# Performance work log

Hardware: AMD Instinct MI355X
Metric: run time of the kernel (lower is better)

The kernel has to match this reference:

```python
import jax, jax.numpy as jnp
import numpy as np
from jax import lax

B, N, C = 8, 100000, 90
H = W = 512
CONF_THR = 0.25
IOU_THR = 0.45
MAX_DET = 100  # fixed-size padded replacement for dynamic per-image NMS output


def setup_inputs() -> dict:
    key = jax.random.key(0)
    k1, k2, k3, k4, k5 = jax.random.split(key, 5)
    # small deltas so exp(dw), exp(dh) stay sane
    regression = jax.random.normal(k1, (B, N, 4), jnp.float32) * 0.1
    # shifted logits so sigmoid scores are mostly below conf_threshold (realistic sparsity)
    classification = jax.random.normal(k2, (B, N, C), jnp.float32) * 2.0 - 4.0
    # anchors in (y1, x1, y2, x2), valid boxes inside a 512x512 canvas
    cy = jax.random.uniform(k3, (1, N), minval=0.0, maxval=float(H))
    cx = jax.random.uniform(k4, (1, N), minval=0.0, maxval=float(W))
    hw = jax.random.uniform(k5, (1, N, 2), minval=16.0, maxval=128.0)
    hh, ww = hw[..., 0], hw[..., 1]
    anchors = jnp.stack([cy - hh / 2, cx - ww / 2, cy + hh / 2, cx + ww / 2], axis=-1)
    imgs = jnp.zeros((B, 3, H, W), jnp.float32)  # only shape (H, W) is used
    return {"regression": regression, "classification": classification,
            "anchors": anchors, "imgs": imgs}


def _bbox_transform(anchors, regression):
    y_c_a = (anchors[..., 0] + anchors[..., 2]) / 2
    x_c_a = (anchors[..., 1] + anchors[..., 3]) / 2
    ha = anchors[..., 2] - anchors[..., 0]
    wa = anchors[..., 3] - anchors[..., 1]
    w = jnp.exp(regression[..., 3]) * wa
    h = jnp.exp(regression[..., 2]) * ha
    y_c = regression[..., 0] * ha + y_c_a
    x_c = regression[..., 1] * wa + x_c_a
    # output in (x1, y1, x2, y2)
    return jnp.stack([x_c - w / 2, y_c - h / 2, x_c + w / 2, y_c + h / 2], axis=-1)


def _clip_boxes(boxes, height, width):
    x = jnp.clip(boxes[..., 0::2], 0.0, float(width))
    y = jnp.clip(boxes[..., 1::2], 0.0, float(height))
    return jnp.stack([x[..., 0], y[..., 0], x[..., 1], y[..., 1]], axis=-1)


def _iou_one_vs_all(box, boxes):
    # box [4], boxes [N,4] in x1y1x2y2
    x1 = jnp.maximum(box[0], boxes[:, 0])
    y1 = jnp.maximum(box[1], boxes[:, 1])
    x2 = jnp.minimum(box[2], boxes[:, 2])
    y2 = jnp.minimum(box[3], boxes[:, 3])
    inter = jnp.clip(x2 - x1, 0.0) * jnp.clip(y2 - y1, 0.0)
    area = (box[2] - box[0]) * (box[3] - box[1])
    areas = (boxes[:, 2] - boxes[:, 0]) * (boxes[:, 3] - boxes[:, 1])
    return inter / (area + areas - inter + 1e-8)


def _process_image(boxes, cls_logits):
    # boxes [N,4], cls_logits [N,C]
    scores_all = jax.nn.sigmoid(cls_logits)
    max_scores = jnp.max(scores_all, axis=1)
    labels = jnp.argmax(scores_all, axis=1)
    # below-threshold anchors get -1 so they can never be selected (== torch pre-NMS filter)
    s0 = jnp.where(max_scores > CONF_THR, max_scores, -1.0)
    s0 = lax.stop_gradient(s0)
    boxes_sg = lax.stop_gradient(boxes)

    def step(sc, _):
        best = jnp.argmax(sc)
        valid = sc[best] > 0.0
        iou = _iou_one_vs_all(boxes_sg[best], boxes_sg)
        sc = jnp.where(valid & (iou > IOU_THR), -1.0, sc)
        sc = sc.at[best].set(-1.0)
        return sc, jnp.where(valid, best, -1)

    _, idx = lax.scan(step, s0, None, length=MAX_DET)  # [MAX_DET] int
    valid = idx >= 0
    idx_safe = jnp.maximum(idx, 0)
    out_scores = jnp.where(valid, max_scores[idx_safe], 0.0)
    out_labels = jnp.where(valid, labels[idx_safe], -1)
    out_boxes = jnp.where(valid[:, None], boxes[idx_safe], 0.0)
    return out_scores, out_labels, out_boxes


def reference(regression, classification, anchors, imgs):
    height, width = imgs.shape[2], imgs.shape[3]
    boxes = _bbox_transform(anchors, regression)          # [B,N,4]
    boxes = _clip_boxes(boxes, height, width)
    scores, labels, det_boxes = jax.vmap(_process_image)(boxes, classification)
    # padded outputs: scores [B,MAX_DET], labels [B,MAX_DET] (-1 = invalid), boxes [B,MAX_DET,4]
    return scores, labels, det_boxes
```

## Files before the change

### kernel.cpp

```cpp
#include <hip/hip_runtime.h>

#define NB 8
#define NA 100000
#define NC 90
#define MAXDET 100
#define KCAND 2048
#define NBINS 4096
#define NBLK 13
#define BLK_ANCH 8000
#define CONF 0.25f
#define IOUT 0.45f

static constexpr size_t OFF_BOX   = 0;
static constexpr size_t OFF_SCORE = OFF_BOX   + (size_t)NB * NA * 16;
static constexpr size_t OFF_LABEL = OFF_SCORE + (size_t)NB * NA * 4;
static constexpr size_t OFF_HROWS = OFF_LABEL + (size_t)NB * NA;
static constexpr size_t OFF_THR   = OFF_HROWS + (size_t)NB * NBLK * NBINS * 4;
static constexpr size_t OFF_CNT   = OFF_THR   + 64;
static constexpr size_t OFF_CKEY  = OFF_CNT   + 64;
static constexpr size_t OFF_CBOX  = OFF_CKEY  + (size_t)NB * KCAND * 8;
static constexpr size_t OFF_CLAB  = OFF_CBOX  + (size_t)NB * KCAND * 16;

__device__ __forceinline__ float4 decode_clip(float4 a, float4 r) {
#pragma clang fp contract(off)
    float yca = (a.x + a.z) * 0.5f;
    float xca = (a.y + a.w) * 0.5f;
    float ha  = a.z - a.x;
    float wa  = a.w - a.y;
    float w   = expf(r.w) * wa;
    float h   = expf(r.z) * ha;
    float yc  = r.x * ha + yca;
    float xc  = r.y * wa + xca;
    float x1  = xc - w * 0.5f, y1 = yc - h * 0.5f;
    float x2  = xc + w * 0.5f, y2 = yc + h * 0.5f;
    x1 = fminf(fmaxf(x1, 0.0f), 512.0f);
    x2 = fminf(fmaxf(x2, 0.0f), 512.0f);
    y1 = fminf(fmaxf(y1, 0.0f), 512.0f);
    y2 = fminf(fmaxf(y2, 0.0f), 512.0f);
    return make_float4(x1, y1, x2, y2);
}

__global__ __launch_bounds__(256) void k_score_box(const float* __restrict__ cls,
                                                   const float* __restrict__ reg,
                                                   const float* __restrict__ anc,
                                                   float4* __restrict__ ws_box,
                                                   float* __restrict__ ws_score,
                                                   unsigned char* __restrict__ ws_label) {
    int tid = threadIdx.x;
    int grp = tid >> 4;
    int lane = tid & 15;
    int a_idx = blockIdx.x * 16 + grp;

    const float* p = cls + (size_t)a_idx * NC;
    unsigned long long best = 0ULL;
#pragma unroll
    for (int t = 0; t < 6; ++t) {
        int j = lane + 16 * t;
        if (j < NC) {
            float x = p[j];
            float s = 1.0f / (1.0f + expf(-x));
            unsigned long long key = ((unsigned long long)__float_as_uint(s) << 32) |
                                     (unsigned long long)(unsigned)(NC - 1 - j);
            if (key > best) best = key;
        }
    }
#pragma unroll
    for (int off = 8; off >= 1; off >>= 1) {
        unsigned long long o = __shfl_xor(best, off, 16);
        if (o > best) best = o;
    }
    if (lane == 0) {
        ws_score[a_idx] = __uint_as_float((unsigned)(best >> 32));
        ws_label[a_idx] = (unsigned char)(NC - 1 - (int)(best & 0xFFFFFFFFu));
    }

    if (tid < 16) {
        int idx = blockIdx.x * 16 + tid;
        int n = idx % NA;
        float4 a = ((const float4*)anc)[n];
        float4 r = ((const float4*)reg)[idx];
        ws_box[idx] = decode_clip(a, r);
    }
}

__global__ __launch_bounds__(256) void k_hist(const float* __restrict__ ws_score,
                                              unsigned* __restrict__ hrows) {
    __shared__ unsigned h[NBINS];
    int b = blockIdx.y, blk = blockIdx.x, tid = threadIdx.x;
    for (int i = tid; i < NBINS; i += 256) h[i] = 0u;
    __syncthreads();
    int base = blk * BLK_ANCH;
    int lim = min(BLK_ANCH, NA - base);
    const float* sc = ws_score + (size_t)b * NA + base;
    for (int i = tid; i < lim; i += 256) {
        float s = sc[i];
        if (s > CONF) {
            int bin = min((int)(s * (float)NBINS), NBINS - 1);
            atomicAdd(&h[bin], 1u);
        }
    }
    __syncthreads();
    unsigned* row = hrows + ((size_t)b * NBLK + blk) * NBINS;
    for (int i = tid; i < NBINS; i += 256) row[i] = h[i];
}

__global__ __launch_bounds__(256) void k_thresh(const unsigned* __restrict__ hrows,
                                                unsigned* __restrict__ thr_bin,
                                                unsigned* __restrict__ cnt) {
    __shared__ unsigned h[NBINS];
    __shared__ unsigned chunk[256];
    __shared__ int bstar;
    int b = blockIdx.x, t = threadIdx.x;
    for (int i = t; i < NBINS; i += 256) {
        unsigned s = 0;
        for (int r = 0; r < NBLK; ++r) s += hrows[((size_t)b * NBLK + r) * NBINS + i];
        h[i] = s;
    }
    if (t == 0) { bstar = NBINS - 1; cnt[b] = 0u; }
    __syncthreads();
    unsigned s = 0;
    for (int j = 0; j < 16; ++j) s += h[t * 16 + j];
    chunk[t] = s;
    __syncthreads();
    unsigned U = 0;
    for (int j = t + 1; j < 256; ++j) U += chunk[j];
    unsigned run = U;
    int cand = NBINS;
    for (int j = 15; j >= 0; --j) {
        run += h[t * 16 + j];
        if (run <= (unsigned)KCAND) cand = t * 16 + j;
    }
    if (cand < NBINS) atomicMin(&bstar, cand);
    __syncthreads();
    if (t == 0) thr_bin[b] = (unsigned)bstar;
}

__global__ __launch_bounds__(256) void k_compact(const float* __restrict__ ws_score,
                                                 const unsigned char* __restrict__ ws_label,
                                                 const float4* __restrict__ ws_box,
                                                 const unsigned* __restrict__ thr_bin,
                                                 unsigned* __restrict__ cnt,
                                                 unsigned long long* __restrict__ ckey,
                                                 float4* __restrict__ cbox,
                                                 int* __restrict__ clab) {
    __shared__ unsigned scan[256];
    __shared__ unsigned base_s;
    int b = blockIdx.y, blk = blockIdx.x, t = threadIdx.x;
    int base = blk * BLK_ANCH;
    int lim = min(BLK_ANCH, NA - base);
    size_t ibase = (size_t)b * NA + base;
    unsigned thr = thr_bin[b];

    unsigned c = 0;
    for (int i = t; i < lim; i += 256) {
        float s = ws_score[ibase + i];
        if (s > CONF) {
            int bin = min((int)(s * (float)NBINS), NBINS - 1);
            if ((unsigned)bin >= thr) c++;
        }
    }
    scan[t] = c;
    __syncthreads();
    for (int off = 1; off < 256; off <<= 1) {
        unsigned v = (t >= off) ? scan[t - off] : 0u;
        __syncthreads();
        scan[t] += v;
        __syncthreads();
    }
    if (t == 255) base_s = atomicAdd(&cnt[b], scan[255]);
    __syncthreads();
    unsigned pos = base_s + scan[t] - c;
    for (int i = t; i < lim; i += 256) {
        float s = ws_score[ibase + i];
        if (s > CONF) {
            int bin = min((int)(s * (float)NBINS), NBINS - 1);
            if ((unsigned)bin >= thr) {
                unsigned p = pos++;
                if (p < (unsigned)KCAND) {
                    int n = base + i;
                    ckey[(size_t)b * KCAND + p] =
                        ((unsigned long long)__float_as_uint(s) << 32) |
                        (unsigned long long)(0xFFFFFFFFu - (unsigned)n);
                    cbox[(size_t)b * KCAND + p] = ws_box[ibase + i];
                    clab[(size_t)b * KCAND + p] = (int)ws_label[ibase + i];
                }
            }
        }
    }
}

__global__ __launch_bounds__(256) void k_nms(const unsigned long long* __restrict__ ckey,
                                             const float4* __restrict__ cbox,
                                             const int* __restrict__ clab,
                                             const unsigned* __restrict__ cnt,
                                             float* __restrict__ out) {
    __shared__ unsigned long long key[KCAND];
    __shared__ float4 box[KCAND];
    __shared__ int lab[KCAND];
    __shared__ unsigned long long bestkey;
    __shared__ float4 bestbox;
    __shared__ int bestlab;
    __shared__ float out_s[MAXDET];
    __shared__ float out_l[MAXDET];
    __shared__ float4 out_b[MAXDET];

    int b = blockIdx.x, t = threadIdx.x;
    unsigned M = min(cnt[b], (unsigned)KCAND);
    for (int j = t; j < KCAND; j += 256) {
        if (j < (int)M) {
            key[j] = ckey[b * KCAND + j];
            box[j] = cbox[b * KCAND + j];
            lab[j] = clab[b * KCAND + j];
        } else {
            key[j] = 0ULL;
        }
    }
    if (t == 0) bestkey = 0ULL;
    __syncthreads();

    for (int k = 0; k < MAXDET; ++k) {
        unsigned long long m = 0ULL;
#pragma unroll
        for (int s = 0; s < KCAND / 256; ++s) {
            unsigned long long v = key[t + s * 256];
            if (v > m) m = v;
        }
#pragma unroll
        for (int off = 32; off >= 1; off >>= 1) {
            unsigned long long o = __shfl_xor(m, off, 64);
            if (o > m) m = o;
        }
        if ((t & 63) == 0) atomicMax(&bestkey, m);
        __syncthreads();
        unsigned long long bk = bestkey;
        if (bk) {
#pragma unroll
            for (int s = 0; s < KCAND / 256; ++s) {
                int j = t + s * 256;
                if (key[j] == bk) {
                    bestbox = box[j];
                    bestlab = lab[j];
                    key[j] = 0ULL;
                }
            }
        }
        __syncthreads();
        if (bk) {
#pragma clang fp contract(off)
            float4 bb = bestbox;
            float areaB = (bb.z - bb.x) * (bb.w - bb.y);
#pragma unroll
            for (int s = 0; s < KCAND / 256; ++s) {
                int j = t + s * 256;
                unsigned long long kj = key[j];
                if (kj) {
                    float4 bj = box[j];
                    float x1 = fmaxf(bb.x, bj.x), y1 = fmaxf(bb.y, bj.y);
                    float x2 = fminf(bb.z, bj.z), y2 = fminf(bb.w, bj.w);
                    float inter = fmaxf(x2 - x1, 0.0f) * fmaxf(y2 - y1, 0.0f);
                    float areaJ = (bj.z - bj.x) * (bj.w - bj.y);
                    float iou = inter / (areaB + areaJ - inter + 1e-8f);
                    if (iou > IOUT) key[j] = 0ULL;
                }
            }
        }
        if (t == 0) {
            if (bk) {
                out_s[k] = __uint_as_float((unsigned)(bk >> 32));
                out_l[k] = (float)bestlab;
                out_b[k] = bestbox;
            } else {
                out_s[k] = 0.0f;
                out_l[k] = -1.0f;
                out_b[k] = make_float4(0.f, 0.f, 0.f, 0.f);
            }
            bestkey = 0ULL;
        }
        __syncthreads();
    }

    if (t < MAXDET) {
        out[b * MAXDET + t] = out_s[t];
        out[NB * MAXDET + b * MAXDET + t] = out_l[t];
    }
    for (int j = t; j < MAXDET * 4; j += 256) {
        int d = j >> 2, c = j & 3;
        float4 bb = out_b[d];
        float v = (c == 0) ? bb.x : (c == 1) ? bb.y : (c == 2) ? bb.z : bb.w;
        out[2 * NB * MAXDET + (size_t)(b * MAXDET + d) * 4 + c] = v;
    }
}

extern "C" void kernel_launch(void* const* d_in, const int* in_sizes, int n_in,
                              void* d_out, int out_size, void* d_ws, size_t ws_size,
                              hipStream_t stream) {
    const float* reg = (const float*)d_in[0];
    const float* cls = (const float*)d_in[1];
    const float* anc = (const float*)d_in[2];

    char* ws = (char*)d_ws;
    float4* ws_box            = (float4*)(ws + OFF_BOX);
    float* ws_score           = (float*)(ws + OFF_SCORE);
    unsigned char* ws_label   = (unsigned char*)(ws + OFF_LABEL);
    unsigned* hrows           = (unsigned*)(ws + OFF_HROWS);
    unsigned* thr_bin         = (unsigned*)(ws + OFF_THR);
    unsigned* cnt             = (unsigned*)(ws + OFF_CNT);
    unsigned long long* ckey  = (unsigned long long*)(ws + OFF_CKEY);
    float4* cbox              = (float4*)(ws + OFF_CBOX);
    int* clab                 = (int*)(ws + OFF_CLAB);

    float* out = (float*)d_out;

    k_score_box<<<NB * NA / 16, 256, 0, stream>>>(cls, reg, anc, ws_box, ws_score, ws_label);
    k_hist<<<dim3(NBLK, NB), 256, 0, stream>>>(ws_score, hrows);
    k_thresh<<<NB, 256, 0, stream>>>(hrows, thr_bin, cnt);
    k_compact<<<dim3(NBLK, NB), 256, 0, stream>>>(ws_score, ws_label, ws_box, thr_bin, cnt,
                                                  ckey, cbox, clab);
    k_nms<<<NB, 256, 0, stream>>>(ckey, cbox, clab, cnt, out);
}
```

Measured before the change: 694.1 us.

## Replace greedy NMS with sorted bitmask NMS and lazy box decode

The score kernel now stages classification rows in shared memory and uses two threads per anchor. Box decoding is moved out of the full pass and done only for the compacted candidates after a bitonic sort. NMS becomes a parallel IoU bitmask build over all candidate pairs, followed by a sequential scan over the sorted mask with double-buffered chunk loads. The aim is to remove the per-anchor decode traffic and the 100 serial argmax rounds. In exchange it adds two kernel launches and a 2048x2048 IoU mask computation.

```diff
diff --git a/kernel.cpp b/kernel.cpp
--- a/kernel.cpp
+++ b/kernel.cpp
@@ -8,18 +8,22 @@
 #define NBINS 4096
 #define NBLK 13
 #define BLK_ANCH 8000
+#define ABLK 128
+#define MASK_WORDS 32
+#define CH_ROWS 64
 #define CONF 0.25f
 #define IOUT 0.45f
 
-static constexpr size_t OFF_BOX   = 0;
-static constexpr size_t OFF_SCORE = OFF_BOX   + (size_t)NB * NA * 16;
+static constexpr size_t OFF_SCORE = 0;
 static constexpr size_t OFF_LABEL = OFF_SCORE + (size_t)NB * NA * 4;
 static constexpr size_t OFF_HROWS = OFF_LABEL + (size_t)NB * NA;
 static constexpr size_t OFF_THR   = OFF_HROWS + (size_t)NB * NBLK * NBINS * 4;
-static constexpr size_t OFF_CNT   = OFF_THR   + 64;
-static constexpr size_t OFF_CKEY  = OFF_CNT   + 64;
-static constexpr size_t OFF_CBOX  = OFF_CKEY  + (size_t)NB * KCAND * 8;
-static constexpr size_t OFF_CLAB  = OFF_CBOX  + (size_t)NB * KCAND * 16;
+static constexpr size_t OFF_CNT   = OFF_THR + 64;
+static constexpr size_t OFF_CKEY  = OFF_CNT + 64;
+static constexpr size_t OFF_SSC   = OFF_CKEY + (size_t)NB * KCAND * 8;
+static constexpr size_t OFF_SLAB  = OFF_SSC + (size_t)NB * KCAND * 4;
+static constexpr size_t OFF_SBOX  = OFF_SLAB + (size_t)NB * KCAND * 4;
+static constexpr size_t OFF_MASK  = OFF_SBOX + (size_t)NB * KCAND * 16;
 
 __device__ __forceinline__ float4 decode_clip(float4 a, float4 r) {
 #pragma clang fp contract(off)
@@ -41,45 +45,32 @@
 }
 
 __global__ __launch_bounds__(256) void k_score_box(const float* __restrict__ cls,
-                                                   const float* __restrict__ reg,
-                                                   const float* __restrict__ anc,
-                                                   float4* __restrict__ ws_box,
                                                    float* __restrict__ ws_score,
                                                    unsigned char* __restrict__ ws_label) {
-    int tid = threadIdx.x;
-    int grp = tid >> 4;
-    int lane = tid & 15;
-    int a_idx = blockIdx.x * 16 + grp;
-
-    const float* p = cls + (size_t)a_idx * NC;
+    __shared__ float tile[ABLK * NC];
+    int t = threadIdx.x;
+    const float4* g4 = (const float4*)(cls + (size_t)blockIdx.x * (ABLK * NC));
+    float4* t4 = (float4*)tile;
+    for (int i = t; i < ABLK * NC / 4; i += 256) t4[i] = g4[i];
+    __syncthreads();
+
+    int la = t >> 1, h = t & 1;
+    const float* row = tile + la * NC + h * 45;
+    int jbase = NC - 1 - h * 45;
     unsigned long long best = 0ULL;
-#pragma unroll
-    for (int t = 0; t < 6; ++t) {
-        int j = lane + 16 * t;
-        if (j < NC) {
-            float x = p[j];
-            float s = 1.0f / (1.0f + expf(-x));
-            unsigned long long key = ((unsigned long long)__float_as_uint(s) << 32) |
-                                     (unsigned long long)(unsigned)(NC - 1 - j);
-            if (key > best) best = key;
-        }
-    }
-#pragma unroll
-    for (int off = 8; off >= 1; off >>= 1) {
-        unsigned long long o = __shfl_xor(best, off, 16);
-        if (o > best) best = o;
-    }
-    if (lane == 0) {
-        ws_score[a_idx] = __uint_as_float((unsigned)(best >> 32));
-        ws_label[a_idx] = (unsigned char)(NC - 1 - (int)(best & 0xFFFFFFFFu));
-    }
-
-    if (tid < 16) {
-        int idx = blockIdx.x * 16 + tid;
-        int n = idx % NA;
-        float4 a = ((const float4*)anc)[n];
-        float4 r = ((const float4*)reg)[idx];
-        ws_box[idx] = decode_clip(a, r);
+    for (int j2 = 0; j2 < 45; ++j2) {
+        float x = row[j2];
+        float s = 1.0f / (1.0f + expf(-x));
+        unsigned long long key = ((unsigned long long)__float_as_uint(s) << 32) |
+                                 (unsigned long long)(unsigned)(jbase - j2);
+        if (key > best) best = key;
+    }
+    unsigned long long o = __shfl_xor(best, 1, 64);
+    if (o > best) best = o;
+    if (h == 0) {
+        int a = blockIdx.x * ABLK + la;
+        ws_score[a] = __uint_as_float((unsigned)(best >> 32));
+        ws_label[a] = (unsigned char)(NC - 1 - (unsigned)(best & 0xFFFFFFFFu));
     }
 }
 
@@ -136,13 +127,9 @@
 }
 
 __global__ __launch_bounds__(256) void k_compact(const float* __restrict__ ws_score,
-                                                 const unsigned char* __restrict__ ws_label,
-                                                 const float4* __restrict__ ws_box,
                                                  const unsigned* __restrict__ thr_bin,
                                                  unsigned* __restrict__ cnt,
-                                                 unsigned long long* __restrict__ ckey,
-                                                 float4* __restrict__ cbox,
-                                                 int* __restrict__ clab) {
+                                                 unsigned long long* __restrict__ ckey) {
     __shared__ unsigned scan[256];
     __shared__ unsigned base_s;
     int b = blockIdx.y, blk = blockIdx.x, t = threadIdx.x;
@@ -181,113 +168,163 @@
                     ckey[(size_t)b * KCAND + p] =
                         ((unsigned long long)__float_as_uint(s) << 32) |
                         (unsigned long long)(0xFFFFFFFFu - (unsigned)n);
-                    cbox[(size_t)b * KCAND + p] = ws_box[ibase + i];
-                    clab[(size_t)b * KCAND + p] = (int)ws_label[ibase + i];
                 }
             }
         }
     }
 }
 
-__global__ __launch_bounds__(256) void k_nms(const unsigned long long* __restrict__ ckey,
-                                             const float4* __restrict__ cbox,
-                                             const int* __restrict__ clab,
-                                             const unsigned* __restrict__ cnt,
-                                             float* __restrict__ out) {
+__global__ __launch_bounds__(256) void k_sortdecode(const unsigned long long* __restrict__ ckey,
+                                                    const unsigned* __restrict__ cnt,
+                                                    const unsigned char* __restrict__ ws_label,
+                                                    const float* __restrict__ reg,
+                                                    const float* __restrict__ anc,
+                                                    float* __restrict__ sscore,
+                                                    int* __restrict__ slab,
+                                                    float4* __restrict__ sbox) {
     __shared__ unsigned long long key[KCAND];
-    __shared__ float4 box[KCAND];
-    __shared__ int lab[KCAND];
-    __shared__ unsigned long long bestkey;
-    __shared__ float4 bestbox;
-    __shared__ int bestlab;
-    __shared__ float out_s[MAXDET];
-    __shared__ float out_l[MAXDET];
-    __shared__ float4 out_b[MAXDET];
-
     int b = blockIdx.x, t = threadIdx.x;
     unsigned M = min(cnt[b], (unsigned)KCAND);
-    for (int j = t; j < KCAND; j += 256) {
-        if (j < (int)M) {
-            key[j] = ckey[b * KCAND + j];
-            box[j] = cbox[b * KCAND + j];
-            lab[j] = clab[b * KCAND + j];
-        } else {
-            key[j] = 0ULL;
-        }
-    }
-    if (t == 0) bestkey = 0ULL;
-    __syncthreads();
-
-    for (int k = 0; k < MAXDET; ++k) {
-        unsigned long long m = 0ULL;
-#pragma unroll
-        for (int s = 0; s < KCAND / 256; ++s) {
-            unsigned long long v = key[t + s * 256];
-            if (v > m) m = v;
-        }
-#pragma unroll
-        for (int off = 32; off >= 1; off >>= 1) {
-            unsigned long long o = __shfl_xor(m, off, 64);
-            if (o > m) m = o;
-        }
-        if ((t & 63) == 0) atomicMax(&bestkey, m);
-        __syncthreads();
-        unsigned long long bk = bestkey;
-        if (bk) {
-#pragma unroll
+    for (int i = t; i < KCAND; i += 256)
+        key[i] = (i < (int)M) ? ckey[(size_t)b * KCAND + i] : 0ULL;
+    __syncthreads();
+    for (int k = 2; k <= KCAND; k <<= 1) {
+        for (int j = k >> 1; j > 0; j >>= 1) {
             for (int s = 0; s < KCAND / 256; ++s) {
-                int j = t + s * 256;
-                if (key[j] == bk) {
-                    bestbox = box[j];
-                    bestlab = lab[j];
-                    key[j] = 0ULL;
+                int p = t + s * 256;
+                int q = p ^ j;
+                if (q > p) {
+                    unsigned long long a = key[p], bb = key[q];
+                    bool desc = ((p & k) == 0);
+                    if (desc ? (a < bb) : (a > bb)) { key[p] = bb; key[q] = a; }
                 }
             }
-        }
-        __syncthreads();
-        if (bk) {
+            __syncthreads();
+        }
+    }
+    for (int i = t; i < KCAND; i += 256) {
+        unsigned long long kk = key[i];
+        size_t o = (size_t)b * KCAND + i;
+        if (kk != 0ULL) {
+            unsigned n = 0xFFFFFFFFu - (unsigned)(kk & 0xFFFFFFFFu);
+            sscore[o] = __uint_as_float((unsigned)(kk >> 32));
+            slab[o] = (int)ws_label[(size_t)b * NA + n];
+            float4 a4 = ((const float4*)anc)[n];
+            float4 r4 = ((const float4*)reg)[(size_t)b * NA + n];
+            sbox[o] = decode_clip(a4, r4);
+        } else {
+            sscore[o] = 0.0f;
+            slab[o] = -1;
+            sbox[o] = make_float4(0.f, 0.f, 0.f, 0.f);
+        }
+    }
+}
+
+__global__ __launch_bounds__(256) void k_mask(const float4* __restrict__ sbox,
+                                              unsigned long long* __restrict__ mask) {
+    __shared__ float4 bx[KCAND];
+    int b = blockIdx.y, t = threadIdx.x;
+    for (int i = t; i < KCAND; i += 256) bx[i] = sbox[(size_t)b * KCAND + i];
+    __syncthreads();
+    int r = t >> 5, w = t & 31;
+    int row = blockIdx.x * 8 + r;
+    float4 rb = bx[row];
+    unsigned long long bits = 0ULL;
+    {
 #pragma clang fp contract(off)
-            float4 bb = bestbox;
-            float areaB = (bb.z - bb.x) * (bb.w - bb.y);
+        float areaR = (rb.z - rb.x) * (rb.w - rb.y);
+        int cbase = w * 64;
+        for (int cc = 0; cc < 64; ++cc) {
+            float4 cb = bx[cbase + cc];
+            float x1 = fmaxf(rb.x, cb.x), y1 = fmaxf(rb.y, cb.y);
+            float x2 = fminf(rb.z, cb.z), y2 = fminf(rb.w, cb.w);
+            float inter = fmaxf(x2 - x1, 0.0f) * fmaxf(y2 - y1, 0.0f);
+            float areaC = (cb.z - cb.x) * (cb.w - cb.y);
+            float iou = inter / (areaR + areaC - inter + 1e-8f);
+            if (iou > IOUT) bits |= (1ULL << cc);
+        }
+    }
+    mask[((size_t)b * KCAND + row) * MASK_WORDS + w] = bits;
+}
+
+__global__ __launch_bounds__(256) void k_scan(const unsigned long long* __restrict__ mask,
+                                              const unsigned* __restrict__ cnt,
+                                              const float* __restrict__ sscore,
+                                              const int* __restrict__ slab,
+                                              const float4* __restrict__ sbox,
+                                              float* __restrict__ out) {
+    __shared__ unsigned long long buf[2][CH_ROWS * MASK_WORDS];
+    __shared__ int picks[MAXDET];
+    __shared__ int npick_s;
+    __shared__ int done_s;
+
+    int b = blockIdx.x, t = threadIdx.x;
+    unsigned M = min(cnt[b], (unsigned)KCAND);
+    const unsigned long long* mbase = mask + (size_t)b * KCAND * MASK_WORDS;
+
+    if (t == 0) { npick_s = 0; done_s = 0; }
+    for (int i = t; i < CH_ROWS * MASK_WORDS; i += 256) buf[0][i] = mbase[i];
+    __syncthreads();
+
+    unsigned long long removed = 0ULL;
+    int npick = 0;
+
+    for (int q = 0; q < KCAND / CH_ROWS; ++q) {
+        int cur = q & 1;
+        bool havepre = (q + 1 < KCAND / CH_ROWS) && !done_s;
+        unsigned long long pre[CH_ROWS * MASK_WORDS / 256];
+        if (havepre) {
+            const unsigned long long* src = mbase + (size_t)(q + 1) * CH_ROWS * MASK_WORDS;
 #pragma unroll
-            for (int s = 0; s < KCAND / 256; ++s) {
-                int j = t + s * 256;
-                unsigned long long kj = key[j];
-                if (kj) {
-                    float4 bj = box[j];
-                    float x1 = fmaxf(bb.x, bj.x), y1 = fmaxf(bb.y, bj.y);
-                    float x2 = fminf(bb.z, bj.z), y2 = fminf(bb.w, bj.w);
-                    float inter = fmaxf(x2 - x1, 0.0f) * fmaxf(y2 - y1, 0.0f);
-                    float areaJ = (bj.z - bj.x) * (bj.w - bj.y);
-                    float iou = inter / (areaB + areaJ - inter + 1e-8f);
-                    if (iou > IOUT) key[j] = 0ULL;
+            for (int s = 0; s < CH_ROWS * MASK_WORDS / 256; ++s) pre[s] = src[t + s * 256];
+        }
+        if (t < 64) {
+            const unsigned long long* ch = buf[cur];
+            int gstart = q * 64;
+            if (gstart < (int)M && npick < MAXDET) {
+                int vg = (int)M - gstart;
+                unsigned long long valid = (vg >= 64) ? ~0ULL : ((1ULL << vg) - 1ULL);
+                while (npick < MAXDET) {
+                    unsigned long long rg = __shfl(removed, q, 64);
+                    unsigned long long free = ~rg & valid;
+                    if (free == 0ULL) break;
+                    int cl = __ffsll((long long)free) - 1;
+                    int c = gstart + cl;
+                    if (t == 0) picks[npick] = c;
+                    npick++;
+                    if (t == q) removed |= (1ULL << cl);
+                    if (t < 32) removed |= ch[cl * MASK_WORDS + t];
                 }
             }
-        }
-        if (t == 0) {
-            if (bk) {
-                out_s[k] = __uint_as_float((unsigned)(bk >> 32));
-                out_l[k] = (float)bestlab;
-                out_b[k] = bestbox;
-            } else {
-                out_s[k] = 0.0f;
-                out_l[k] = -1.0f;
-                out_b[k] = make_float4(0.f, 0.f, 0.f, 0.f);
+            if (t == 0) {
+                npick_s = npick;
+                done_s = (npick >= MAXDET || (q + 1) * CH_ROWS >= (int)M) ? 1 : 0;
             }
-            bestkey = 0ULL;
+        }
+        if (havepre) {
+#pragma unroll
+            for (int s = 0; s < CH_ROWS * MASK_WORDS / 256; ++s)
+                buf[1 - cur][t + s * 256] = pre[s];
         }
         __syncthreads();
-    }
-
-    if (t < MAXDET) {
-        out[b * MAXDET + t] = out_s[t];
-        out[NB * MAXDET + b * MAXDET + t] = out_l[t];
-    }
-    for (int j = t; j < MAXDET * 4; j += 256) {
-        int d = j >> 2, c = j & 3;
-        float4 bb = out_b[d];
-        float v = (c == 0) ? bb.x : (c == 1) ? bb.y : (c == 2) ? bb.z : bb.w;
-        out[2 * NB * MAXDET + (size_t)(b * MAXDET + d) * 4 + c] = v;
+        if (done_s) break;
+    }
+
+    __syncthreads();
+    int np = npick_s;
+    for (int k = t; k < MAXDET; k += 256) {
+        float sc = 0.0f, lb = -1.0f;
+        float4 bb = make_float4(0.f, 0.f, 0.f, 0.f);
+        if (k < np) {
+            int i = picks[k];
+            size_t o = (size_t)b * KCAND + i;
+            sc = sscore[o];
+            lb = (float)slab[o];
+            bb = sbox[o];
+        }
+        out[b * MAXDET + k] = sc;
+        out[NB * MAXDET + b * MAXDET + k] = lb;
+        ((float4*)(out + 2 * NB * MAXDET))[b * MAXDET + k] = bb;
     }
 }
 
@@ -299,22 +336,24 @@
     const float* anc = (const float*)d_in[2];
 
     char* ws = (char*)d_ws;
-    float4* ws_box            = (float4*)(ws + OFF_BOX);
     float* ws_score           = (float*)(ws + OFF_SCORE);
     unsigned char* ws_label   = (unsigned char*)(ws + OFF_LABEL);
     unsigned* hrows           = (unsigned*)(ws + OFF_HROWS);
     unsigned* thr_bin         = (unsigned*)(ws + OFF_THR);
     unsigned* cnt             = (unsigned*)(ws + OFF_CNT);
     unsigned long long* ckey  = (unsigned long long*)(ws + OFF_CKEY);
-    float4* cbox              = (float4*)(ws + OFF_CBOX);
-    int* clab                 = (int*)(ws + OFF_CLAB);
+    float* sscore             = (float*)(ws + OFF_SSC);
+    int* slab                 = (int*)(ws + OFF_SLAB);
+    float4* sbox              = (float4*)(ws + OFF_SBOX);
+    unsigned long long* maskp = (unsigned long long*)(ws + OFF_MASK);
 
     float* out = (float*)d_out;
 
-    k_score_box<<<NB * NA / 16, 256, 0, stream>>>(cls, reg, anc, ws_box, ws_score, ws_label);
+    k_score_box<<<NB * NA / ABLK, 256, 0, stream>>>(cls, ws_score, ws_label);
     k_hist<<<dim3(NBLK, NB), 256, 0, stream>>>(ws_score, hrows);
     k_thresh<<<NB, 256, 0, stream>>>(hrows, thr_bin, cnt);
-    k_compact<<<dim3(NBLK, NB), 256, 0, stream>>>(ws_score, ws_label, ws_box, thr_bin, cnt,
-                                                  ckey, cbox, clab);
-    k_nms<<<NB, 256, 0, stream>>>(ckey, cbox, clab, cnt, out);
-}
+    k_compact<<<dim3(NBLK, NB), 256, 0, stream>>>(ws_score, thr_bin, cnt, ckey);
+    k_sortdecode<<<NB, 256, 0, stream>>>(ckey, cnt, ws_label, reg, anc, sscore, slab, sbox);
+    k_mask<<<dim3(KCAND / 8, NB), 256, 0, stream>>>(sbox, maskp);
+    k_scan<<<NB, 256, 0, stream>>>(maskp, cnt, sscore, slab, sbox, out);
+}
```

After: 608.0 us. -12.4%, faster.
